# Kernel tuning notes

Hardware: AMD Instinct MI355X
Metric: run time of the kernel (lower is better)

## Reference

```python
import jax, jax.numpy as jnp
import numpy as np

B, S, E, H, F = 4, 2048, 1024, 16, 4096
D = E // H
EPS = 1e-5


def setup_inputs() -> dict:
    key = jax.random.key(0)
    ks = jax.random.split(key, 12)
    sc_e = 1.0 / np.sqrt(E)
    sc_f = 1.0 / np.sqrt(F)
    inp = {
        'x': jax.random.normal(ks[0], (B, S, E), jnp.float32),
        'mask': jnp.tril(jnp.ones((S, S), jnp.int32))[None, None],  # causal [1,1,S,S]
        'ln1_g': jnp.ones((E,), jnp.float32),
        'ln1_b': jnp.zeros((E,), jnp.float32),
        'Wq': jax.random.normal(ks[1], (E, E), jnp.float32) * sc_e,
        'bq': jnp.zeros((E,), jnp.float32),
        'Wk': jax.random.normal(ks[2], (E, E), jnp.float32) * sc_e,
        'bk': jnp.zeros((E,), jnp.float32),
        'Wv': jax.random.normal(ks[3], (E, E), jnp.float32) * sc_e,
        'bv': jnp.zeros((E,), jnp.float32),
        'Wo': jax.random.normal(ks[4], (E, E), jnp.float32) * sc_e,
        'bo': jnp.zeros((E,), jnp.float32),
        'ln2_g': jnp.ones((E,), jnp.float32),
        'ln2_b': jnp.zeros((E,), jnp.float32),
        'W1': jax.random.normal(ks[5], (F, E), jnp.float32) * sc_e,
        'b1': jnp.zeros((F,), jnp.float32),
        'W2': jax.random.normal(ks[6], (E, F), jnp.float32) * sc_f,
        'b2': jnp.zeros((E,), jnp.float32),
    }
    return inp


def _ln(x, g, b):
    m = jnp.mean(x, axis=-1, keepdims=True)
    v = jnp.mean(jnp.square(x - m), axis=-1, keepdims=True)
    return (x - m) * jax.lax.rsqrt(v + EPS) * g + b


def _attn(h, mask, Wq, bq, Wk, bk, Wv, bv, Wo, bo):
    b, s, _ = h.shape
    q = (h @ Wq.T + bq).reshape(b, s, H, D)
    k = (h @ Wk.T + bk).reshape(b, s, H, D)
    v = (h @ Wv.T + bv).reshape(b, s, H, D)
    scores = jnp.einsum('bqhd,bkhd->bhqk', q, k) / np.sqrt(D)
    scores = jnp.where(mask == 0, -jnp.inf, scores)
    w = jax.nn.softmax(scores, axis=-1)
    ctx = jnp.einsum('bhqk,bkhd->bqhd', w, v).reshape(b, s, E)
    return ctx @ Wo.T + bo


def reference(x, mask, ln1_g, ln1_b, Wq, bq, Wk, bk, Wv, bv, Wo, bo,
              ln2_g, ln2_b, W1, b1, W2, b2):
    x = x + _attn(_ln(x, ln1_g, ln1_b), mask, Wq, bq, Wk, bk, Wv, bv, Wo, bo)
    h = _ln(x, ln2_g, ln2_b)
    ffn = jax.nn.gelu(h @ W1.T + b1, approximate=False) @ W2.T + b2
    return x + ffn
```

## Files before the change

kernel.cpp:

```cpp
#include <hip/hip_runtime.h>
#include <cstdint>
#include <cstddef>

#define E_DIM 1024
#define F_DIM 4096
#define S_LEN 2048
#define NB    4
#define NH    16
#define HD    64
#define MROWS 8192

typedef __bf16 bf16x8 __attribute__((ext_vector_type(8)));
typedef float  f32x4  __attribute__((ext_vector_type(4)));

struct alignas(16) f4 { float x, y, z, w; };
__device__ __forceinline__ f4 ld4(const float* p){ return *(const f4*)p; }

__device__ __forceinline__ unsigned short f2bf(float f){
  union { float f; unsigned int u; } c; c.f = f;
  unsigned int u = c.u;
  return (unsigned short)((u + 0x7FFFu + ((u >> 16) & 1u)) >> 16);
}

__global__ void cvt_kernel(const float* __restrict__ in, unsigned short* __restrict__ out,
                           int n, float scale){
  int i = (blockIdx.x * 256 + threadIdx.x) * 4;
  if (i >= n) return;
  f4 f = ld4(in + i);
  ushort4 o;
  o.x = f2bf(f.x * scale); o.y = f2bf(f.y * scale);
  o.z = f2bf(f.z * scale); o.w = f2bf(f.w * scale);
  *(ushort4*)(out + i) = o;
}

__global__ void bias_cat(const float* __restrict__ bq, const float* __restrict__ bk,
                         const float* __restrict__ bv, float* __restrict__ out, float qsc){
  int i = blockIdx.x * 256 + threadIdx.x;
  if (i >= 3 * E_DIM) return;
  float v = (i < E_DIM) ? bq[i] * qsc : (i < 2 * E_DIM ? bk[i - E_DIM] : bv[i - 2 * E_DIM]);
  out[i] = v;
}

__global__ __launch_bounds__(256) void ln_kernel(const float* __restrict__ in,
                                                 const float* __restrict__ g,
                                                 const float* __restrict__ b,
                                                 unsigned short* __restrict__ out){
  const int row = blockIdx.x;
  const int t = threadIdx.x;
  const float* xr = in + (size_t)row * E_DIM;
  f4 xv = ld4(xr + t * 4);
  float s  = xv.x + xv.y + xv.z + xv.w;
  float ss = xv.x*xv.x + xv.y*xv.y + xv.z*xv.z + xv.w*xv.w;
  #pragma unroll
  for (int o = 1; o < 64; o <<= 1){ s += __shfl_xor(s, o); ss += __shfl_xor(ss, o); }
  __shared__ float sa[4], sb[4];
  if ((t & 63) == 0){ sa[t >> 6] = s; sb[t >> 6] = ss; }
  __syncthreads();
  s  = sa[0] + sa[1] + sa[2] + sa[3];
  ss = sb[0] + sb[1] + sb[2] + sb[3];
  const float mean = s * (1.0f / E_DIM);
  const float var  = ss * (1.0f / E_DIM) - mean * mean;
  const float rstd = rsqrtf(var + 1e-5f);
  f4 gv = ld4(g + t * 4);
  f4 bv = ld4(b + t * 4);
  ushort4 o;
  o.x = f2bf((xv.x - mean) * rstd * gv.x + bv.x);
  o.y = f2bf((xv.y - mean) * rstd * gv.y + bv.y);
  o.z = f2bf((xv.z - mean) * rstd * gv.z + bv.z);
  o.w = f2bf((xv.w - mean) * rstd * gv.w + bv.w);
  *(ushort4*)(out + (size_t)row * E_DIM + t * 4) = o;
}

__device__ __forceinline__ void async_cp16(const unsigned short* g, unsigned short* l){
  __builtin_amdgcn_global_load_lds((const __attribute__((address_space(1))) unsigned int*)g,
                                   (__attribute__((address_space(3)))       unsigned int*)l,
                                   16, 0, 0);
}

__device__ __forceinline__ unsigned lds_off(const void* p){
  return (unsigned)(size_t)(const __attribute__((address_space(3))) char*)p;
}
__device__ __forceinline__ bf16x8 ds_read128(unsigned addr){
  bf16x8 r;
  asm volatile("ds_read_b128 %0, %1" : "=v"(r) : "v"(addr));
  return r;
}

template<int EPI>
__global__ __launch_bounds__(256) void gemm_bt(const unsigned short* __restrict__ A,
                                               const unsigned short* __restrict__ W,
                                               const float* __restrict__ bias,
                                               const float* __restrict__ res,
                                               void* __restrict__ outp,
                                               int M, int N, int K){
  __shared__ unsigned short As[128 * 64];
  __shared__ unsigned short Bs[128 * 64];
  const int bn = blockIdx.x, bm = blockIdx.y;
  const int tid = threadIdx.x;
  const int wv = tid >> 6, lane = tid & 63;
  const int lr = lane & 15, qd = lane >> 4;
  const int wm = (wv >> 1) * 64, wn = (wv & 1) * 64;

  f32x4 acc[4][4];
  #pragma unroll
  for (int mt = 0; mt < 4; ++mt)
    #pragma unroll
    for (int nt = 0; nt < 4; ++nt)
      acc[mt][nt] = f32x4{0.f, 0.f, 0.f, 0.f};

  int soff[4];
  int srow[4];
  #pragma unroll
  for (int it = 0; it < 4; ++it){
    const int cc = tid + it * 256;
    srow[it] = cc >> 3;
    soff[it] = (((cc & 7) ^ (srow[it] & 7))) * 8;
  }
  const unsigned short* Abase = A + (size_t)(bm * 128) * K;
  const unsigned short* Wbase = W + (size_t)(bn * 128) * K;

  for (int k0 = 0; k0 < K; k0 += 64){
    __syncthreads();
    #pragma unroll
    for (int it = 0; it < 4; ++it){
      async_cp16(Abase + (size_t)srow[it] * K + k0 + soff[it], &As[(tid + it * 256) * 8]);
      async_cp16(Wbase + (size_t)srow[it] * K + k0 + soff[it], &Bs[(tid + it * 256) * 8]);
    }
    __builtin_amdgcn_s_waitcnt(0);
    __syncthreads();

    #pragma unroll
    for (int kk = 0; kk < 2; ++kk){
      bf16x8 af[4], bf[4];
      #pragma unroll
      for (int mt = 0; mt < 4; ++mt){
        const int fr = wm + mt * 16 + lr;
        af[mt] = *(const bf16x8*)&As[fr * 64 + (((kk * 4 + qd) ^ (fr & 7))) * 8];
      }
      #pragma unroll
      for (int nt = 0; nt < 4; ++nt){
        const int fr = wn + nt * 16 + lr;
        bf[nt] = *(const bf16x8*)&Bs[fr * 64 + (((kk * 4 + qd) ^ (fr & 7))) * 8];
      }
      #pragma unroll
      for (int mt = 0; mt < 4; ++mt)
        #pragma unroll
        for (int nt = 0; nt < 4; ++nt)
          acc[mt][nt] = __builtin_amdgcn_mfma_f32_16x16x32_bf16(af[mt], bf[nt], acc[mt][nt], 0, 0, 0);
    }
  }

  #pragma unroll
  for (int mt = 0; mt < 4; ++mt){
    #pragma unroll
    for (int r = 0; r < 4; ++r){
      const int gm = bm * 128 + wm + mt * 16 + qd * 4 + r;
      const size_t rowoff = (size_t)gm * N;
      #pragma unroll
      for (int nt = 0; nt < 4; ++nt){
        const int gn = bn * 128 + wn + nt * 16 + lr;
        float v = acc[mt][nt][r] + bias[gn];
        if constexpr (EPI == 1) v = 0.5f * v * (1.0f + erff(v * 0.70710678118654752f));
        if constexpr (EPI == 2) ((float*)outp)[rowoff + gn] = v + res[rowoff + gn];
        else                    ((unsigned short*)outp)[rowoff + gn] = f2bf(v);
      }
    }
  }
}

#define VMW4() asm volatile("s_waitcnt vmcnt(4)" ::: "memory")
#define VMW0() asm volatile("s_waitcnt vmcnt(0)" ::: "memory")
#define BAR()  __builtin_amdgcn_s_barrier()

template<int EPI>
__global__ __launch_bounds__(512, 2) void gemm256(const unsigned short* __restrict__ A,
                                                  const unsigned short* __restrict__ W,
                                                  const float* __restrict__ bias,
                                                  unsigned short* __restrict__ outp,
                                                  int M, int N, int K){
  __shared__ unsigned short lds[2][2][256 * 64];
  const int bn = blockIdx.x, bm = blockIdx.y;
  const int tid = threadIdx.x;
  const int lane = tid & 63;
  const int wv = tid >> 6;
  const int lr = lane & 15, qd = lane >> 4;
  const int wm = wv >> 2, wn = wv & 3;
  const int NT = K >> 6;

  f32x4 acc[2][2][4][2];
  #pragma unroll
  for (int a = 0; a < 2; ++a)
    #pragma unroll
    for (int b = 0; b < 2; ++b)
      #pragma unroll
      for (int c = 0; c < 4; ++c)
        #pragma unroll
        for (int d = 0; d < 2; ++d)
          acc[a][b][c][d] = f32x4{0.f, 0.f, 0.f, 0.f};

  const int srow = tid >> 3;
  const int scol = ((tid & 7) ^ (srow & 7)) * 8;
  const unsigned short* Ab = A + (size_t)(bm * 256 + srow) * K + scol;
  const unsigned short* Wb = W + (size_t)(bn * 256 + srow) * K + scol;

#define STAGE_A(bufi, h, kt) do{ \
    async_cp16(Ab + (size_t)((h)*128     ) * K + (size_t)(kt) * 64, &lds[bufi][0][((h)*128     ) * 64 + tid * 8]); \
    async_cp16(Ab + (size_t)((h)*128 + 64) * K + (size_t)(kt) * 64, &lds[bufi][0][((h)*128 + 64) * 64 + tid * 8]); \
  }while(0)
#define STAGE_B(bufi, h, kt) do{ \
    async_cp16(Wb + (size_t)((h)*128     ) * K + (size_t)(kt) * 64, &lds[bufi][1][((h)*128     ) * 64 + tid * 8]); \
    async_cp16(Wb + (size_t)((h)*128 + 64) * K + (size_t)(kt) * 64, &lds[bufi][1][((h)*128 + 64) * 64 + tid * 8]); \
  }while(0)

  const int sw0 = ((qd    ) ^ (lr & 7)) * 8;
  const int sw1 = ((qd + 4) ^ (lr & 7)) * 8;
  const unsigned LB = lds_off(&lds[0][0][0]);
  const unsigned aA0 = LB +         (wm * 64 + lr) * 128 + sw0 * 2;
  const unsigned aA1 = LB +         (wm * 64 + lr) * 128 + sw1 * 2;
  const unsigned aB0 = LB + 32768 + (wn * 32 + lr) * 128 + sw0 * 2;
  const unsigned aB1 = LB + 32768 + (wn * 32 + lr) * 128 + sw1 * 2;

  bf16x8 af[4][2], b0[2][2], b1[2][2];

#define LDA(bufi, mh) do{ \
    _Pragma("unroll") \
    for (int mt = 0; mt < 4; ++mt){ \
      const unsigned d_ = (bufi) * 65536u + (mh) * 16384u + mt * 2048u; \
      af[mt][0] = ds_read128(aA0 + d_); \
      af[mt][1] = ds_read128(aA1 + d_); \
    } }while(0)
#define LDB(bufi, nh, dst) do{ \
    _Pragma("unroll") \
    for (int nt = 0; nt < 2; ++nt){ \
      const unsigned d_ = (bufi) * 65536u + (nh) * 16384u + nt * 2048u; \
      dst[nt][0] = ds_read128(aB0 + d_); \
      dst[nt][1] = ds_read128(aB1 + d_); \
    } }while(0)
#define MMA(mh, nh, bfr) do{ \
    asm volatile("s_waitcnt lgkmcnt(0)" ::: "memory"); \
    __builtin_amdgcn_sched_barrier(0); \
    __builtin_amdgcn_s_setprio(1); \
    _Pragma("unroll") \
    for (int kk = 0; kk < 2; ++kk) \
      _Pragma("unroll") \
      for (int mt = 0; mt < 4; ++mt) \
        _Pragma("unroll") \
        for (int nt = 0; nt < 2; ++nt) \
          acc[mh][nh][mt][nt] = __builtin_amdgcn_mfma_f32_16x16x32_bf16(af[mt][kk], bfr[nt][kk], acc[mh][nh][mt][nt], 0, 0, 0); \
    __builtin_amdgcn_s_setprio(0); \
    __builtin_amdgcn_sched_barrier(0); \
  }while(0)

  STAGE_A(0, 0, 0); STAGE_B(0, 1, 0); STAGE_A(0, 1, 0); STAGE_B(0, 0, 0);
  STAGE_A(1, 0, 1); STAGE_B(1, 1, 1);
  VMW4(); BAR();

  for (int t = 0; t < NT; t += 2){
    const bool s2 = (t + 2) < NT, s3 = (t + 3) < NT;
    LDA(0, 0); LDB(0, 0, b0);
    STAGE_A(1, 1, t + 1);
    BAR(); MMA(0, 0, b0); BAR();
    LDB(0, 1, b1);
    STAGE_B(1, 0, t + 1);
    BAR(); MMA(0, 1, b1); BAR();
    LDA(0, 1);
    if (s2) STAGE_A(0, 0, t + 2);
    BAR(); MMA(1, 1, b1); BAR();
    if (s2) STAGE_B(0, 1, t + 2);
    BAR(); MMA(1, 0, b0);
    if (s2) { VMW4(); } else { VMW0(); }
    BAR();
    LDA(1, 0); LDB(1, 0, b0);
    if (s2) STAGE_A(0, 1, t + 2);
    BAR(); MMA(0, 0, b0); BAR();
    LDB(1, 1, b1);
    if (s2) STAGE_B(0, 0, t + 2);
    BAR(); MMA(0, 1, b1); BAR();
    LDA(1, 1);
    if (s3) STAGE_A(1, 0, t + 3);
    BAR(); MMA(1, 1, b1); BAR();
    if (s3) STAGE_B(1, 1, t + 3);
    BAR(); MMA(1, 0, b0);
    VMW4();
    BAR();
  }

  #pragma unroll
  for (int mh = 0; mh < 2; ++mh)
    #pragma unroll
    for (int nh = 0; nh < 2; ++nh)
      #pragma unroll
      for (int mt = 0; mt < 4; ++mt){
        const int gm0 = bm * 256 + mh * 128 + wm * 64 + mt * 16 + qd * 4;
        #pragma unroll
        for (int r = 0; r < 4; ++r){
          const size_t rowoff = (size_t)(gm0 + r) * N;
          #pragma unroll
          for (int nt = 0; nt < 2; ++nt){
            const int gn = bn * 256 + nh * 128 + wn * 32 + nt * 16 + lr;
            float v = acc[mh][nh][mt][nt][r] + bias[gn];
            if constexpr (EPI == 1) v = 0.5f * v * (1.0f + erff(v * 0.70710678118654752f));
            outp[rowoff + gn] = f2bf(v);
          }
        }
      }
#undef STAGE_A
#undef STAGE_B
#undef LDA
#undef LDB
#undef MMA
}

__global__ __launch_bounds__(256) void vtrans(const unsigned short* __restrict__ QKV,
                                              unsigned short* __restrict__ Vt){
  __shared__ unsigned short Ts[64 * 66];
  const int st = blockIdx.x;
  const int h = blockIdx.y, b = blockIdx.z;
  const int tid = threadIdx.x;
  const size_t srcbase = (size_t)(b * S_LEN + st * 64) * 3072 + 2 * E_DIM + h * HD;
  #pragma unroll
  for (int it = 0; it < 4; ++it){
    const int ch = tid + it * 256;
    const int row = ch >> 4, c4 = (ch & 15) * 4;
    *(ushort4*)&Ts[row * 66 + c4] = *(const ushort4*)(QKV + srcbase + (size_t)row * 3072 + c4);
  }
  __syncthreads();
  const size_t dstbase = (size_t)((b * NH + h) * HD) * S_LEN + st * 64;
  #pragma unroll
  for (int it = 0; it < 4; ++it){
    const int ch = tid + it * 256;
    const int d = ch >> 4, t4 = (ch & 15) * 4;
    ushort4 o;
    o.x = Ts[(t4 + 0) * 66 + d];
    o.y = Ts[(t4 + 1) * 66 + d];
    o.z = Ts[(t4 + 2) * 66 + d];
    o.w = Ts[(t4 + 3) * 66 + d];
    *(ushort4*)&Vt[dstbase + (size_t)d * S_LEN + t4] = o;
  }
}

#define AST 72
__global__ __launch_bounds__(256) void attn_mfma(const unsigned short* __restrict__ QKV,
                                                 const unsigned short* __restrict__ Vt,
                                                 unsigned short* __restrict__ Om){
  __shared__ unsigned short Ks[64 * AST];
  __shared__ unsigned short Vs[64 * AST];
  __shared__ unsigned short Ps[64 * AST];
  const int pairi = blockIdx.x;
  const int h = blockIdx.y, b = blockIdx.z;
  const int tid = threadIdx.x;
  const int w = tid >> 6, lane = tid & 63;
  const int lr = lane & 15, qd = lane >> 4;
  const size_t row0 = (size_t)b * S_LEN;
  const int qcol = h * HD;
  const int kcol = E_DIM + h * HD;
  const unsigned short* Vtb = Vt + (size_t)((b * NH + h) * HD) * S_LEN;

  bf16x8 ones;
  #pragma unroll
  for (int j = 0; j < 8; ++j) ones[j] = (__bf16)1.0f;

  for (int ph = 0; ph < 2; ++ph){
    const int qb_t = ph ? (31 - pairi) : pairi;
    const int q0 = qb_t * 64 + w * 16;

    bf16x8 qf[2];
    #pragma unroll
    for (int kk = 0; kk < 2; ++kk)
      qf[kk] = *(const bf16x8*)(QKV + (row0 + q0 + lr) * 3072 + qcol + kk * 32 + qd * 8);

    f32x4 accd[4];
    #pragma unroll
    for (int dt = 0; dt < 4; ++dt) accd[dt] = f32x4{0.f, 0.f, 0.f, 0.f};
    f32x4 lacc = f32x4{0.f, 0.f, 0.f, 0.f};

    for (int kt = 0; kt <= qb_t; ++kt){
      __syncthreads();
      #pragma unroll
      for (int it = 0; it < 2; ++it){
        const int ch = tid + it * 256;
        const int r_ = ch >> 3, c8 = (ch & 7) * 8;
        *(uint4*)&Ks[r_ * AST + c8] = *(const uint4*)(QKV + (row0 + kt * 64 + r_) * 3072 + kcol + c8);
        *(uint4*)&Vs[r_ * AST + c8] = *(const uint4*)(Vtb + (size_t)r_ * S_LEN + kt * 64 + c8);
      }
      __syncthreads();

      f32x4 s[4];
      #pragma unroll
      for (int nt = 0; nt < 4; ++nt) s[nt] = f32x4{0.f, 0.f, 0.f, 0.f};
      #pragma unroll
      for (int kk = 0; kk < 2; ++kk){
        bf16x8 kf[4];
        #pragma unroll
        for (int nt = 0; nt < 4; ++nt)
          kf[nt] = *(const bf16x8*)&Ks[(nt * 16 + lr) * AST + kk * 32 + qd * 8];
        #pragma unroll
        for (int nt = 0; nt < 4; ++nt)
          s[nt] = __builtin_amdgcn_mfma_f32_16x16x32_bf16(qf[kk], kf[nt], s[nt], 0, 0, 0);
      }
      if (kt == qb_t){
        #pragma unroll
        for (int nt = 0; nt < 4; ++nt)
          #pragma unroll
          for (int r = 0; r < 4; ++r){
            const int q  = q0 + qd * 4 + r;
            const int ky = kt * 64 + nt * 16 + lr;
            if (ky > q) s[nt][r] = -3e38f;
          }
      }
      #pragma unroll
      for (int nt = 0; nt < 4; ++nt)
        #pragma unroll
        for (int r = 0; r < 4; ++r){
          union { float f; unsigned u; } cc;
          cc.f = exp2f(s[nt][r]);
          Ps[(w * 16 + qd * 4 + r) * AST + nt * 16 + lr] = (unsigned short)((cc.u + 0x8000u) >> 16);
        }
      __builtin_amdgcn_s_waitcnt(0xc07f);
      #pragma unroll
      for (int kk = 0; kk < 2; ++kk){
        bf16x8 pf = *(const bf16x8*)&Ps[(w * 16 + lr) * AST + kk * 32 + qd * 8];
        bf16x8 vf[4];
        #pragma unroll
        for (int dt = 0; dt < 4; ++dt)
          vf[dt] = *(const bf16x8*)&Vs[(dt * 16 + lr) * AST + kk * 32 + qd * 8];
        #pragma unroll
        for (int dt = 0; dt < 4; ++dt)
          accd[dt] = __builtin_amdgcn_mfma_f32_16x16x32_bf16(pf, vf[dt], accd[dt], 0, 0, 0);
        lacc = __builtin_amdgcn_mfma_f32_16x16x32_bf16(pf, ones, lacc, 0, 0, 0);
      }
    }

    #pragma unroll
    for (int r = 0; r < 4; ++r){
      const float inv = 1.0f / lacc[r];
      const size_t ro = (row0 + q0 + qd * 4 + r) * E_DIM + qcol;
      #pragma unroll
      for (int dt = 0; dt < 4; ++dt)
        Om[ro + dt * 16 + lr] = f2bf(accd[dt][r] * inv);
    }
  }
}

extern "C" void kernel_launch(void* const* d_in, const int* in_sizes, int n_in,
                              void* d_out, int out_size, void* d_ws, size_t ws_size,
                              hipStream_t stream){
  const float* x    = (const float*)d_in[0];
  const float* ln1g = (const float*)d_in[2];
  const float* ln1b = (const float*)d_in[3];
  const float* Wq   = (const float*)d_in[4];
  const float* bq   = (const float*)d_in[5];
  const float* Wk   = (const float*)d_in[6];
  const float* bk   = (const float*)d_in[7];
  const float* Wv   = (const float*)d_in[8];
  const float* bv   = (const float*)d_in[9];
  const float* Wo   = (const float*)d_in[10];
  const float* bo   = (const float*)d_in[11];
  const float* ln2g = (const float*)d_in[12];
  const float* ln2b = (const float*)d_in[13];
  const float* W1   = (const float*)d_in[14];
  const float* b1   = (const float*)d_in[15];
  const float* W2   = (const float*)d_in[16];
  const float* b2   = (const float*)d_in[17];

  char* ws = (char*)d_ws;
  const size_t MB = 1024 * 1024;
  unsigned short* Wqkv_b = (unsigned short*)(ws + 0 * MB);
  unsigned short* Wo_b   = (unsigned short*)(ws + 6 * MB);
  unsigned short* W1_b   = (unsigned short*)(ws + 8 * MB);
  unsigned short* W2_b   = (unsigned short*)(ws + 16 * MB);
  unsigned short* qkvb   = (unsigned short*)(ws + 24 * MB);
  float*          bqkv   = (float*)(ws + 72 * MB);
  unsigned short* Vt_g   = (unsigned short*)(ws + 72 * MB);
  unsigned short* lnb    = (unsigned short*)(ws + 88 * MB);
  float*          xres   = (float*)(ws + 104 * MB);
  unsigned short* ffn1   = (unsigned short*)(ws + 24 * MB);
  unsigned short* ctxb   = lnb;

  const float QSC = 0.125f * 1.4426950408889634f;

  cvt_kernel<<<1024, 256, 0, stream>>>(Wq, Wqkv_b,                   E_DIM * E_DIM, QSC);
  cvt_kernel<<<1024, 256, 0, stream>>>(Wk, Wqkv_b + E_DIM * E_DIM,   E_DIM * E_DIM, 1.0f);
  cvt_kernel<<<1024, 256, 0, stream>>>(Wv, Wqkv_b + 2 * E_DIM * E_DIM, E_DIM * E_DIM, 1.0f);
  cvt_kernel<<<1024, 256, 0, stream>>>(Wo, Wo_b, E_DIM * E_DIM, 1.0f);
  cvt_kernel<<<4096, 256, 0, stream>>>(W1, W1_b, F_DIM * E_DIM, 1.0f);
  cvt_kernel<<<4096, 256, 0, stream>>>(W2, W2_b, F_DIM * E_DIM, 1.0f);
  bias_cat<<<12, 256, 0, stream>>>(bq, bk, bv, bqkv, QSC);

  ln_kernel<<<MROWS, 256, 0, stream>>>(x, ln1g, ln1b, lnb);

  gemm256<0><<<dim3(3 * E_DIM / 256, MROWS / 256), 512, 0, stream>>>(
      lnb, Wqkv_b, bqkv, qkvb, MROWS, 3 * E_DIM, E_DIM);

  vtrans<<<dim3(S_LEN / 64, NH, NB), 256, 0, stream>>>(qkvb, Vt_g);

  attn_mfma<<<dim3(16, NH, NB), 256, 0, stream>>>(qkvb, Vt_g, ctxb);

  gemm_bt<2><<<dim3(E_DIM / 128, MROWS / 128), 256, 0, stream>>>(
      ctxb, Wo_b, bo, x, xres, MROWS, E_DIM, E_DIM);

  ln_kernel<<<MROWS, 256, 0, stream>>>(xres, ln2g, ln2b, lnb);

  gemm256<1><<<dim3(F_DIM / 256, MROWS / 256), 512, 0, stream>>>(
      lnb, W1_b, b1, ffn1, MROWS, F_DIM, E_DIM);

  gemm_bt<2><<<dim3(E_DIM / 128, MROWS / 128), 256, 0, stream>>>(
      ffn1, W2_b, b2, xres, (float*)d_out, MROWS, E_DIM, F_DIM);
}
```

Measured before the change: 562.6 us.

## Restructure gemm256 main loop into deeper software pipeline with fewer barriers

Reworks the 256x256 GEMM main loop so LDS fragment reads for the next MMA are issued before the current MMA, stage loads are reordered, and one barrier per MMA phase replaces the two used before. It keeps more global loads in flight (vmcnt 8 instead of 4) and peels the final iteration into an explicit drain epilogue with a graded vmcnt wait sequence. The aim is to hide global and LDS latency behind MFMA work and cut barrier stalls. This depends on buffer reuse staying correct across the new ordering, and it gives the scheduler less slack.

```diff
diff --git a/kernel.cpp b/kernel.cpp
--- a/kernel.cpp
+++ b/kernel.cpp
@@ -168,9 +168,10 @@
   }
 }
 
-#define VMW4() asm volatile("s_waitcnt vmcnt(4)" ::: "memory")
-#define VMW0() asm volatile("s_waitcnt vmcnt(0)" ::: "memory")
 #define BAR()  __builtin_amdgcn_s_barrier()
+#define VMW(n) asm volatile("s_waitcnt vmcnt(" #n ")" ::: "memory")
+#define WAITK() do{ asm volatile("s_waitcnt lgkmcnt(0)" ::: "memory"); \
+                    __builtin_amdgcn_sched_barrier(0); }while(0)
 
 template<int EPI>
 __global__ __launch_bounds__(512, 2) void gemm256(const unsigned short* __restrict__ A,
@@ -237,8 +238,6 @@
       dst[nt][1] = ds_read128(aB1 + d_); \
     } }while(0)
 #define MMA(mh, nh, bfr) do{ \
-    asm volatile("s_waitcnt lgkmcnt(0)" ::: "memory"); \
-    __builtin_amdgcn_sched_barrier(0); \
     __builtin_amdgcn_s_setprio(1); \
     _Pragma("unroll") \
     for (int kk = 0; kk < 2; ++kk) \
@@ -251,38 +250,74 @@
     __builtin_amdgcn_sched_barrier(0); \
   }while(0)
 
-  STAGE_A(0, 0, 0); STAGE_B(0, 1, 0); STAGE_A(0, 1, 0); STAGE_B(0, 0, 0);
-  STAGE_A(1, 0, 1); STAGE_B(1, 1, 1);
-  VMW4(); BAR();
-
-  for (int t = 0; t < NT; t += 2){
-    const bool s2 = (t + 2) < NT, s3 = (t + 3) < NT;
+  STAGE_A(0, 0, 0); STAGE_B(0, 0, 0); STAGE_B(0, 1, 0); STAGE_A(0, 1, 0);
+  STAGE_A(1, 0, 1); STAGE_B(1, 0, 1); STAGE_B(1, 1, 1);
+  VMW(8); BAR();
+  LDA(0, 0); LDB(0, 0, b0);
+
+  int t = 0;
+  for (; t + 3 < NT; t += 2){
+    WAITK(); MMA(0, 0, b0);
+    LDB(0, 1, b1);
+    STAGE_A(1, 1, t + 1);
+    VMW(8); BAR();
+    WAITK(); MMA(0, 1, b1);
+    LDA(0, 1);
+    STAGE_A(0, 0, t + 2);
+    VMW(8); BAR();
+    WAITK(); MMA(1, 1, b1);
+    STAGE_B(0, 0, t + 2);
+    VMW(8); BAR();
+    WAITK(); MMA(1, 0, b0);
+    LDA(1, 0); LDB(1, 0, b0);
+    STAGE_B(0, 1, t + 2);
+    VMW(8); BAR();
+    WAITK(); MMA(0, 0, b0);
+    LDB(1, 1, b1);
+    STAGE_A(0, 1, t + 2);
+    VMW(8); BAR();
+    WAITK(); MMA(0, 1, b1);
+    LDA(1, 1);
+    STAGE_A(1, 0, t + 3);
+    VMW(8); BAR();
+    WAITK(); MMA(1, 1, b1);
+    STAGE_B(1, 0, t + 3);
+    VMW(8); BAR();
+    WAITK(); MMA(1, 0, b0);
     LDA(0, 0); LDB(0, 0, b0);
+    STAGE_B(1, 1, t + 3);
+    VMW(8); BAR();
+  }
+
+  {
+    WAITK(); MMA(0, 0, b0);
+    LDB(0, 1, b1);
     STAGE_A(1, 1, t + 1);
-    BAR(); MMA(0, 0, b0); BAR();
-    LDB(0, 1, b1);
-    STAGE_B(1, 0, t + 1);
-    BAR(); MMA(0, 1, b1); BAR();
+    VMW(8); BAR();
+
+    WAITK(); MMA(0, 1, b1);
     LDA(0, 1);
-    if (s2) STAGE_A(0, 0, t + 2);
-    BAR(); MMA(1, 1, b1); BAR();
-    if (s2) STAGE_B(0, 1, t + 2);
-    BAR(); MMA(1, 0, b0);
-    if (s2) { VMW4(); } else { VMW0(); }
+    VMW(6); BAR();
+
+    WAITK(); MMA(1, 1, b1);
+    VMW(4); BAR();
+
+    WAITK(); MMA(1, 0, b0);
+    LDA(1, 0); LDB(1, 0, b0);
+    VMW(2); BAR();
+
+    WAITK(); MMA(0, 0, b0);
+    LDB(1, 1, b1);
+    VMW(0); BAR();
+
+    WAITK(); MMA(0, 1, b1);
+    LDA(1, 1);
     BAR();
-    LDA(1, 0); LDB(1, 0, b0);
-    if (s2) STAGE_A(0, 1, t + 2);
-    BAR(); MMA(0, 0, b0); BAR();
-    LDB(1, 1, b1);
-    if (s2) STAGE_B(0, 0, t + 2);
-    BAR(); MMA(0, 1, b1); BAR();
-    LDA(1, 1);
-    if (s3) STAGE_A(1, 0, t + 3);
-    BAR(); MMA(1, 1, b1); BAR();
-    if (s3) STAGE_B(1, 1, t + 3);
-    BAR(); MMA(1, 0, b0);
-    VMW4();
+
+    WAITK(); MMA(1, 1, b1);
     BAR();
+
+    WAITK(); MMA(1, 0, b0);
   }
 
   #pragma unroll
```

Result: slower. 777.7 us (+38.2%).
